# Kernel optimization log

Measured on AMD Instinct MI355X. Metric: run time of the kernel, lower is better.

The kernel has to match this reference:

```python
import jax, jax.numpy as jnp
import numpy as np


def setup_inputs() -> dict:
    key = jax.random.key(0)
    k1, k2, k3 = jax.random.split(key, 3)
    B, T, H = 64, 512, 1024
    return {
        "encoder_out": jax.random.normal(k1, (B, T, H), dtype=jnp.float32),
        "W_ih": jax.random.normal(k2, (3 * H, H), dtype=jnp.float32) * (1.0 / np.sqrt(H)),
        "W_hh": jax.random.normal(k3, (3 * H, H), dtype=jnp.float32) * (1.0 / np.sqrt(H)),
        "b_ih": jnp.zeros((3 * H,), dtype=jnp.float32),
        "b_hh": jnp.zeros((3 * H,), dtype=jnp.float32),
    }


def reference(encoder_out, W_ih, W_hh, b_ih, b_hh):
    # PyTorch GRUCell semantics; gate order in stacked weights is (r, z, n).
    B, T, H = encoder_out.shape

    # Batch the input-to-hidden projection across all timesteps: [B,T,3H]
    x_proj = jnp.einsum("bth,gh->btg", encoder_out, W_ih) + b_ih
    x_proj_t = jnp.swapaxes(x_proj, 0, 1)  # [T, B, 3H] for scan

    W_hh_T = W_hh.T  # [H, 3H]

    def step(h, xp):
        # recurrent projection: [B, 3H]
        h_proj = h @ W_hh_T + b_hh
        xr, xz, xn = jnp.split(xp, 3, axis=-1)
        hr, hz, hn = jnp.split(h_proj, 3, axis=-1)
        r = jax.nn.sigmoid(xr + hr)
        z = jax.nn.sigmoid(xz + hz)
        n = jnp.tanh(xn + r * hn)
        h_new = (1.0 - z) * n + z * h
        return h_new, h_new

    h0 = jnp.zeros((B, H), dtype=encoder_out.dtype)
    _, h_seq = jax.lax.scan(step, h0, x_proj_t)  # [T, B, H]
    return jnp.swapaxes(h_seq, 0, 1)  # [B, T, H]
```

## Files before the change

### kernel.cpp

```cpp
#include <hip/hip_runtime.h>
#include <hip/hip_bf16.h>


typedef short bf16x8 __attribute__((ext_vector_type(8)));
typedef float f32x4 __attribute__((ext_vector_type(4)));

#define NB 64
#define NT 512
#define NH 1024
#define NG 3072

static __device__ __forceinline__ float bf2f(unsigned short u) {
    unsigned int x = ((unsigned int)u) << 16;
    float f;
    __builtin_memcpy(&f, &x, sizeof(f));
    return f;
}
static __device__ __forceinline__ unsigned short f2bf(float f) {
    unsigned int x;
    __builtin_memcpy(&x, &f, sizeof(x));
    x += 0x7fffu + ((x >> 16) & 1u);
    return (unsigned short)(x >> 16);
}

static __device__ __forceinline__ f32x4 mfma16(bf16x8 a, bf16x8 b, f32x4 c) {
    return __builtin_amdgcn_mfma_f32_16x16x32_bf16(a, b, c, 0, 0, 0);
}

#define GLD16(gp, lp) __builtin_amdgcn_global_load_lds( \
    (const __attribute__((address_space(1))) void*)(gp), \
    (__attribute__((address_space(3))) void*)(lp), 16, 0, 0)

__global__ void k_fill_sentinel(float* __restrict__ o, long n) {
    long i = (long)blockIdx.x * blockDim.x + threadIdx.x;
    if (i < n) o[i] = 12345.0f;
}

__global__ void k_convert(const float* __restrict__ in, unsigned short* __restrict__ o, int n) {
    int i = blockIdx.x * blockDim.x + threadIdx.x;
    if (i < n) o[i] = f2bf(in[i]);
}

__global__ void k_convert_enc(const float* __restrict__ enc, unsigned short* __restrict__ o) {
    long i = (long)blockIdx.x * blockDim.x + threadIdx.x;
    if (i >= (long)NB * NT * NH) return;
    int h = (int)(i % NH);
    long bt = i / NH;
    int t = (int)(bt % NT);
    int b = (int)(bt / NT);
    o[((long)t * NB + b) * NH + h] = f2bf(enc[i]);
}

#define SYNC_WORDS (4 * NB * NH / 2 + 128)
__global__ void k_init_sync(unsigned int* __restrict__ base) {
    int i = blockIdx.x * blockDim.x + threadIdx.x;
    if (i < SYNC_WORDS) base[i] = 0u;
}

__global__ __launch_bounds__(256) void k_xproj(
    const unsigned short* __restrict__ X,
    const unsigned short* __restrict__ W,
    const float* __restrict__ bias,
    unsigned short* __restrict__ xp)
{
    __shared__ unsigned short As[128 * 32];
    __shared__ unsigned short Bs[128 * 32];

    const int tid  = threadIdx.x;
    const int lane = tid & 63;
    const int wv   = tid >> 6;
    const int l16  = lane & 15;
    const int lq   = lane >> 4;
    const int wr   = wv >> 1;
    const int wc   = wv & 1;
    const int n0   = blockIdx.x * 128;
    const int m0   = blockIdx.y * 128;

    f32x4 acc[4][4];
#pragma unroll
    for (int mi = 0; mi < 4; ++mi)
#pragma unroll
        for (int nj = 0; nj < 4; ++nj) acc[mi][nj] = (f32x4){0.f, 0.f, 0.f, 0.f};

    const int r0 = tid >> 2;
    const int c0e = (tid & 3) * 8;
    const int r1 = (256 + tid) >> 2;

    for (int k0 = 0; k0 < NH; k0 += 32) {
        GLD16(X + (size_t)(m0 + r0) * NH + k0 + c0e, &As[tid * 8]);
        GLD16(X + (size_t)(m0 + r1) * NH + k0 + c0e, &As[(256 + tid) * 8]);
        GLD16(W + (size_t)(n0 + r0) * NH + k0 + c0e, &Bs[tid * 8]);
        GLD16(W + (size_t)(n0 + r1) * NH + k0 + c0e, &Bs[(256 + tid) * 8]);
        __syncthreads();

        bf16x8 a[4], b[4];
#pragma unroll
        for (int mi = 0; mi < 4; ++mi)
            a[mi] = *(const bf16x8*)&As[(wr * 64 + mi * 16 + l16) * 32 + lq * 8];
#pragma unroll
        for (int nj = 0; nj < 4; ++nj)
            b[nj] = *(const bf16x8*)&Bs[(wc * 64 + nj * 16 + l16) * 32 + lq * 8];
#pragma unroll
        for (int mi = 0; mi < 4; ++mi)
#pragma unroll
            for (int nj = 0; nj < 4; ++nj)
                acc[mi][nj] = mfma16(a[mi], b[nj], acc[mi][nj]);
        __syncthreads();
    }

#pragma unroll
    for (int nj = 0; nj < 4; ++nj) {
        int n = n0 + wc * 64 + nj * 16 + l16;
        float bv = bias[n];
        int g   = n >> 10;
        int u   = n & 1023;
        int ugb = u >> 5;
        int ui  = u & 31;
#pragma unroll
        for (int mi = 0; mi < 4; ++mi) {
#pragma unroll
            for (int i = 0; i < 4; ++i) {
                int m = m0 + wr * 64 + mi * 16 + lq * 4 + i;
                int t = m >> 6;
                int b = m & 63;
                xp[(((long)t * 32 + ugb) * 64 + b) * 96 + g * 32 + ui] = f2bf(acc[mi][nj][i] + bv);
            }
        }
    }
}

__global__ __launch_bounds__(512, 1) void k_scan(
    const unsigned short* __restrict__ Whh,
    const float* __restrict__ bhh,
    const unsigned short* __restrict__ xp,
    unsigned short* __restrict__ hring,
    unsigned* __restrict__ flags,
    float* __restrict__ out)
{
    const int tid  = threadIdx.x;
    const int lane = tid & 63;
    const int wv   = tid >> 6;
    const int l16  = lane & 15;
    const int lq   = lane >> 4;
    const int bid  = blockIdx.x;
    const int mg   = bid >> 5;
    const int ug   = bid & 31;
    const int m0   = mg * 16;
    const int u0   = ug * 32;
    const int kc0  = wv * 128;

    bf16x8 Bf[3][2][4];
#pragma unroll
    for (int g = 0; g < 3; ++g)
#pragma unroll
        for (int f = 0; f < 2; ++f)
#pragma unroll
            for (int ks = 0; ks < 4; ++ks)
                Bf[g][f][ks] = *(const bf16x8*)(Whh + (long)(g * NH + u0 + f * 16 + l16) * NH + kc0 + ks * 32 + lq * 8);
#pragma unroll
    for (int g = 0; g < 3; ++g)
#pragma unroll
        for (int f = 0; f < 2; ++f)
#pragma unroll
            for (int ks = 0; ks < 4; ++ks)
                asm volatile("" : "+v"(Bf[g][f][ks]));

    const int u_loc = tid & 31;
    const int b_loc = tid >> 5;
    const int b_own = m0 + b_loc;
    const int u_own = u0 + u_loc;
    float bh[3];
#pragma unroll
    for (int g = 0; g < 3; ++g) bh[g] = bhh[g * NH + u_own];
    float hf = 0.0f;

    const int lane_t = (b_loc >> 2) * 16 + (u_loc & 15);
    const int i_t    = b_loc & 3;
    const int shalf  = (u_loc >> 4) * 3;

    __shared__ f32x4 red[8][6][64];

    for (int t = 0; t < NT; ++t) {
        const int slot_r = (t + 3) & 3;
        const int slot_w = t & 3;

        const unsigned short* xpp = xp + (((long)t * 32 + ug) * 64 + b_own) * 96;
        float xr = bf2f(xpp[u_loc]);
        float xz = bf2f(xpp[32 + u_loc]);
        float xn = bf2f(xpp[64 + u_loc]);

        if (t > 0) {
            if (wv == 0) {
                const unsigned* fp = flags + mg * 32 + (lane & 31);
                for (;;) {
                    unsigned fv;
                    asm volatile("global_load_dword %0, %1, off sc0 sc1\n\ts_waitcnt vmcnt(0)"
                                 : "=v"(fv) : "v"(fp) : "memory");
                    if (__all(fv >= (unsigned)t)) break;
                }
            }
            __syncthreads();
        }

        const unsigned short* hp = hring + ((slot_r * NB + m0 + l16) * NH + kc0 + lq * 8);
        bf16x8 av[4];
        asm volatile(
            "global_load_dwordx4 %0, %4, off sc0 sc1\n\t"
            "global_load_dwordx4 %1, %4, off offset:64 sc0 sc1\n\t"
            "global_load_dwordx4 %2, %4, off offset:128 sc0 sc1\n\t"
            "global_load_dwordx4 %3, %4, off offset:192 sc0 sc1\n\t"
            "s_waitcnt vmcnt(0)"
            : "=&v"(av[0]), "=&v"(av[1]), "=&v"(av[2]), "=&v"(av[3])
            : "v"(hp) : "memory");

        f32x4 acc[2][3];
#pragma unroll
        for (int f = 0; f < 2; ++f)
#pragma unroll
            for (int g = 0; g < 3; ++g) acc[f][g] = (f32x4){0.f, 0.f, 0.f, 0.f};
#pragma unroll
        for (int ks = 0; ks < 4; ++ks)
#pragma unroll
            for (int f = 0; f < 2; ++f)
#pragma unroll
                for (int g = 0; g < 3; ++g)
                    acc[f][g] = mfma16(av[ks], Bf[g][f][ks], acc[f][g]);

#pragma unroll
        for (int f = 0; f < 2; ++f)
#pragma unroll
            for (int g = 0; g < 3; ++g) red[wv][f * 3 + g][lane] = acc[f][g];
        __syncthreads();

        float pre[3];
#pragma unroll
        for (int g = 0; g < 3; ++g) {
            float s = 0.0f;
#pragma unroll
            for (int w = 0; w < 8; ++w) s += red[w][shalf + g][lane_t][i_t];
            pre[g] = s + bh[g];
        }

        float r = 1.0f / (1.0f + __expf(-(xr + pre[0])));
        float z = 1.0f / (1.0f + __expf(-(xz + pre[1])));
        float narg = xn + r * pre[2];
        float nval = 1.0f - 2.0f / (__expf(2.0f * narg) + 1.0f);
        float hnew = (1.0f - z) * nval + z * hf;
        hf = hnew;

        {
            unsigned short* hw = hring + (slot_w * NB + b_own) * NH + u_own;
            unsigned hv = (unsigned)f2bf(hnew);
            asm volatile("global_store_short %0, %1, off sc0 sc1"
                         :: "v"(hw), "v"(hv) : "memory");
        }
        asm volatile("s_waitcnt vmcnt(0)" ::: "memory");
        __syncthreads();
        if (tid == 0) {
            unsigned fv = (unsigned)(t + 1);
            asm volatile("global_store_dword %0, %1, off sc0 sc1"
                         :: "v"(flags + mg * 32 + ug), "v"(fv) : "memory");
        }
        out[((long)b_own * NT + t) * NH + u_own] = hnew;
    }
}

extern "C" void kernel_launch(void* const* d_in, const int* in_sizes, int n_in,
                              void* d_out, int out_size, void* d_ws, size_t ws_size,
                              hipStream_t stream) {
    const float* enc = (const float*)d_in[0];
    const float* Wih = (const float*)d_in[1];
    const float* Whh = (const float*)d_in[2];
    const float* bih = (const float*)d_in[3];
    const float* bhh = (const float*)d_in[4];
    float* out = (float*)d_out;

    char* p = (char*)d_ws;
    unsigned short* enc_t = (unsigned short*)p; p += (size_t)NT * NB * NH * 2;
    unsigned short* xp    = (unsigned short*)p; p += (size_t)NT * NB * NG * 2;
    unsigned short* wih_b = (unsigned short*)p; p += (size_t)NG * NH * 2;
    unsigned short* whh_b = (unsigned short*)p; p += (size_t)NG * NH * 2;
    size_t need = (size_t)(p - (char*)d_ws);

    unsigned short* hring = enc_t;
    unsigned* flags = (unsigned*)(hring + (size_t)4 * NB * NH);

    if (ws_size < need) {
        long n = (long)out_size;
        k_fill_sentinel<<<(int)((n + 255) / 256), 256, 0, stream>>>(out, n);
        return;
    }

    {
        int n = NG * NH;
        k_convert<<<(n + 255) / 256, 256, 0, stream>>>(Wih, wih_b, n);
        k_convert<<<(n + 255) / 256, 256, 0, stream>>>(Whh, whh_b, n);
        long ne = (long)NB * NT * NH;
        k_convert_enc<<<(int)((ne + 255) / 256), 256, 0, stream>>>(enc, enc_t);
    }

    {
        dim3 grid(NG / 128, (NT * NB) / 128);
        k_xproj<<<grid, 256, 0, stream>>>(enc_t, wih_b, bih, xp);
    }

    k_init_sync<<<(SYNC_WORDS + 255) / 256, 256, 0, stream>>>((unsigned*)hring);

    k_scan<<<128, 512, 0, stream>>>(whh_b, bhh, xp, hring, flags, out);
}
```

Before: 2.307 ms.

## Fuse input projection into the scan kernel and overlap it via per-tile flags

Launches one kernel of 256 blocks. The first 128 blocks compute the input projection, reading fp32 encoder data straight from memory and converting it to bf16 in place, then raise a per-tile done flag. The other 128 blocks run the recurrent scan and poll those flags before consuming each timestep. This removes the separate encoder transpose/convert pass and the xproj launch, and lets the projection overlap the latency-bound recurrence. The cost is that projection blocks use a smaller 128x128 tile with single-buffered LDS and no reuse across repeats. Correctness also depends on both block groups being resident at the same time, since the scan blocks spin on flags.

```diff
diff --git a/kernel.cpp b/kernel.cpp
--- a/kernel.cpp
+++ b/kernel.cpp
@@ -41,113 +41,123 @@
     if (i < n) o[i] = f2bf(in[i]);
 }
 
-__global__ void k_convert_enc(const float* __restrict__ enc, unsigned short* __restrict__ o) {
-    long i = (long)blockIdx.x * blockDim.x + threadIdx.x;
-    if (i >= (long)NB * NT * NH) return;
-    int h = (int)(i % NH);
-    long bt = i / NH;
-    int t = (int)(bt % NT);
-    int b = (int)(bt / NT);
-    o[((long)t * NB + b) * NH + h] = f2bf(enc[i]);
-}
-
-#define SYNC_WORDS (4 * NB * NH / 2 + 128)
+#define SYNC_WORDS (4 * NB * NH / 2 + 128 + 256)
 __global__ void k_init_sync(unsigned int* __restrict__ base) {
     int i = blockIdx.x * blockDim.x + threadIdx.x;
     if (i < SYNC_WORDS) base[i] = 0u;
 }
 
-__global__ __launch_bounds__(256) void k_xproj(
-    const unsigned short* __restrict__ X,
-    const unsigned short* __restrict__ W,
-    const float* __restrict__ bias,
-    unsigned short* __restrict__ xp)
-{
-    __shared__ unsigned short As[128 * 32];
-    __shared__ unsigned short Bs[128 * 32];
-
-    const int tid  = threadIdx.x;
-    const int lane = tid & 63;
-    const int wv   = tid >> 6;
-    const int l16  = lane & 15;
-    const int lq   = lane >> 4;
-    const int wr   = wv >> 1;
-    const int wc   = wv & 1;
-    const int n0   = blockIdx.x * 128;
-    const int m0   = blockIdx.y * 128;
-
-    f32x4 acc[4][4];
-#pragma unroll
-    for (int mi = 0; mi < 4; ++mi)
-#pragma unroll
-        for (int nj = 0; nj < 4; ++nj) acc[mi][nj] = (f32x4){0.f, 0.f, 0.f, 0.f};
-
-    const int r0 = tid >> 2;
-    const int c0e = (tid & 3) * 8;
-    const int r1 = (256 + tid) >> 2;
-
-    for (int k0 = 0; k0 < NH; k0 += 32) {
-        GLD16(X + (size_t)(m0 + r0) * NH + k0 + c0e, &As[tid * 8]);
-        GLD16(X + (size_t)(m0 + r1) * NH + k0 + c0e, &As[(256 + tid) * 8]);
-        GLD16(W + (size_t)(n0 + r0) * NH + k0 + c0e, &Bs[tid * 8]);
-        GLD16(W + (size_t)(n0 + r1) * NH + k0 + c0e, &Bs[(256 + tid) * 8]);
-        __syncthreads();
-
-        bf16x8 a[4], b[4];
-#pragma unroll
-        for (int mi = 0; mi < 4; ++mi)
-            a[mi] = *(const bf16x8*)&As[(wr * 64 + mi * 16 + l16) * 32 + lq * 8];
-#pragma unroll
-        for (int nj = 0; nj < 4; ++nj)
-            b[nj] = *(const bf16x8*)&Bs[(wc * 64 + nj * 16 + l16) * 32 + lq * 8];
-#pragma unroll
-        for (int mi = 0; mi < 4; ++mi)
-#pragma unroll
-            for (int nj = 0; nj < 4; ++nj)
-                acc[mi][nj] = mfma16(a[mi], b[nj], acc[mi][nj]);
-        __syncthreads();
-    }
-
-#pragma unroll
-    for (int nj = 0; nj < 4; ++nj) {
-        int n = n0 + wc * 64 + nj * 16 + l16;
-        float bv = bias[n];
-        int g   = n >> 10;
-        int u   = n & 1023;
-        int ugb = u >> 5;
-        int ui  = u & 31;
-#pragma unroll
-        for (int mi = 0; mi < 4; ++mi) {
-#pragma unroll
-            for (int i = 0; i < 4; ++i) {
-                int m = m0 + wr * 64 + mi * 16 + lq * 4 + i;
-                int t = m >> 6;
-                int b = m & 63;
-                xp[(((long)t * 32 + ugb) * 64 + b) * 96 + g * 32 + ui] = f2bf(acc[mi][nj][i] + bv);
-            }
-        }
-    }
-}
-
-__global__ __launch_bounds__(512, 1) void k_scan(
+__global__ __launch_bounds__(512, 1) void k_fused(
+    const unsigned short* __restrict__ Wih,
     const unsigned short* __restrict__ Whh,
+    const float* __restrict__ bih,
     const float* __restrict__ bhh,
-    const unsigned short* __restrict__ xp,
+    const float* __restrict__ enc,
+    unsigned short* __restrict__ xp,
     unsigned short* __restrict__ hring,
     unsigned* __restrict__ flags,
+    unsigned* __restrict__ xpdone,
     float* __restrict__ out)
 {
+    __shared__ char lds_raw[49152];
+
     const int tid  = threadIdx.x;
     const int lane = tid & 63;
     const int wv   = tid >> 6;
     const int l16  = lane & 15;
     const int lq   = lane >> 4;
     const int bid  = blockIdx.x;
-    const int mg   = bid >> 5;
-    const int ug   = bid & 31;
-    const int m0   = mg * 16;
-    const int u0   = ug * 32;
-    const int kc0  = wv * 128;
+
+    if (bid < 128) {
+        unsigned short* As = (unsigned short*)lds_raw;
+        unsigned short* Bs = (unsigned short*)(lds_raw + 8192);
+        const int wr = wv >> 2;
+        const int wc = wv & 3;
+        const int r  = tid >> 2;
+        const int ce = (tid & 3) * 8;
+
+        for (int rep = 0; rep < 2; ++rep) {
+            const int mt = bid + rep * 128;
+            const int m0 = mt * 128;
+            const int ma = m0 + r;
+            const float* agp = enc + ((size_t)(ma & 63) * NT + (ma >> 6)) * NH + ce;
+
+            for (int nt = 0; nt < 24; ++nt) {
+                const int n0 = nt * 128;
+                f32x4 acc[4][2];
+#pragma unroll
+                for (int mi = 0; mi < 4; ++mi)
+#pragma unroll
+                    for (int nj = 0; nj < 2; ++nj) acc[mi][nj] = (f32x4){0.f, 0.f, 0.f, 0.f};
+
+                for (int k0 = 0; k0 < NH; k0 += 32) {
+                    {
+                        float4 fa = *(const float4*)(agp + k0);
+                        float4 fb = *(const float4*)(agp + k0 + 4);
+                        union { unsigned short s[8]; bf16x8 v; } cv;
+                        cv.s[0] = f2bf(fa.x); cv.s[1] = f2bf(fa.y);
+                        cv.s[2] = f2bf(fa.z); cv.s[3] = f2bf(fa.w);
+                        cv.s[4] = f2bf(fb.x); cv.s[5] = f2bf(fb.y);
+                        cv.s[6] = f2bf(fb.z); cv.s[7] = f2bf(fb.w);
+                        *(bf16x8*)&As[r * 32 + ce] = cv.v;
+                    }
+                    GLD16(Wih + (size_t)(n0 + r) * NH + k0 + ce, &Bs[tid * 8]);
+                    __syncthreads();
+
+                    bf16x8 a[4], b[2];
+#pragma unroll
+                    for (int mi = 0; mi < 4; ++mi)
+                        a[mi] = *(const bf16x8*)&As[(wr * 64 + mi * 16 + l16) * 32 + lq * 8];
+#pragma unroll
+                    for (int nj = 0; nj < 2; ++nj)
+                        b[nj] = *(const bf16x8*)&Bs[(wc * 32 + nj * 16 + l16) * 32 + lq * 8];
+#pragma unroll
+                    for (int mi = 0; mi < 4; ++mi)
+#pragma unroll
+                        for (int nj = 0; nj < 2; ++nj)
+                            acc[mi][nj] = mfma16(a[mi], b[nj], acc[mi][nj]);
+                    __syncthreads();
+                }
+
+#pragma unroll
+                for (int nj = 0; nj < 2; ++nj) {
+                    int n = n0 + wc * 32 + nj * 16 + l16;
+                    float bv = bih[n];
+                    int g   = n >> 10;
+                    int u   = n & 1023;
+                    int ugb = u >> 5;
+                    int ui  = u & 31;
+#pragma unroll
+                    for (int mi = 0; mi < 4; ++mi) {
+#pragma unroll
+                        for (int i = 0; i < 4; ++i) {
+                            int m = m0 + wr * 64 + mi * 16 + lq * 4 + i;
+                            int t = m >> 6;
+                            int b = m & 63;
+                            xp[(((long)t * 32 + ugb) * 64 + b) * 96 + g * 32 + ui] =
+                                f2bf(acc[mi][nj][i] + bv);
+                        }
+                    }
+                }
+            }
+            __threadfence();
+            __syncthreads();
+            if (tid == 0) {
+                unsigned one = 1u;
+                asm volatile("global_store_dword %0, %1, off sc0 sc1"
+                             :: "v"(xpdone + mt), "v"(one) : "memory");
+            }
+        }
+        return;
+    }
+
+    f32x4 (*red)[6][64] = (f32x4(*)[6][64])lds_raw;
+    const int sb  = bid - 128;
+    const int mg  = sb >> 5;
+    const int ug  = sb & 31;
+    const int m0  = mg * 16;
+    const int u0  = ug * 32;
+    const int kc0 = wv * 128;
 
     bf16x8 Bf[3][2][4];
 #pragma unroll
@@ -178,40 +188,42 @@
     const int i_t    = b_loc & 3;
     const int shalf  = (u_loc >> 4) * 3;
 
-    __shared__ f32x4 red[8][6][64];
+    const unsigned* fp_h = flags + mg * 32 + wv * 4 + (lane & 3);
 
     for (int t = 0; t < NT; ++t) {
         const int slot_r = (t + 3) & 3;
         const int slot_w = t & 3;
 
-        const unsigned short* xpp = xp + (((long)t * 32 + ug) * 64 + b_own) * 96;
-        float xr = bf2f(xpp[u_loc]);
-        float xz = bf2f(xpp[32 + u_loc]);
-        float xn = bf2f(xpp[64 + u_loc]);
-
-        if (t > 0) {
-            if (wv == 0) {
-                const unsigned* fp = flags + mg * 32 + (lane & 31);
-                for (;;) {
-                    unsigned fv;
-                    asm volatile("global_load_dword %0, %1, off sc0 sc1\n\ts_waitcnt vmcnt(0)"
-                                 : "=v"(fv) : "v"(fp) : "memory");
-                    if (__all(fv >= (unsigned)t)) break;
-                }
+        {
+            const unsigned tgt = (lane < 4) ? (unsigned)t : 1u;
+            const unsigned* pp = (lane < 4) ? fp_h : (xpdone + (t >> 1));
+            for (;;) {
+                unsigned fv;
+                asm volatile("global_load_dword %0, %1, off sc0 sc1\n\ts_waitcnt vmcnt(0)"
+                             : "=v"(fv) : "v"(pp) : "memory");
+                if (__all(fv >= tgt)) break;
             }
-            __syncthreads();
-        }
-
+        }
+
+        const unsigned short* xaddr = xp + (((long)t * 32 + ug) * 64 + b_own) * 96 + u_loc;
         const unsigned short* hp = hring + ((slot_r * NB + m0 + l16) * NH + kc0 + lq * 8);
+        unsigned xv0, xv1, xv2;
         bf16x8 av[4];
         asm volatile(
-            "global_load_dwordx4 %0, %4, off sc0 sc1\n\t"
-            "global_load_dwordx4 %1, %4, off offset:64 sc0 sc1\n\t"
-            "global_load_dwordx4 %2, %4, off offset:128 sc0 sc1\n\t"
-            "global_load_dwordx4 %3, %4, off offset:192 sc0 sc1\n\t"
+            "global_load_ushort %0, %7, off sc0 sc1\n\t"
+            "global_load_ushort %1, %7, off offset:64 sc0 sc1\n\t"
+            "global_load_ushort %2, %7, off offset:128 sc0 sc1\n\t"
+            "global_load_dwordx4 %3, %8, off sc0 sc1\n\t"
+            "global_load_dwordx4 %4, %8, off offset:64 sc0 sc1\n\t"
+            "global_load_dwordx4 %5, %8, off offset:128 sc0 sc1\n\t"
+            "global_load_dwordx4 %6, %8, off offset:192 sc0 sc1\n\t"
             "s_waitcnt vmcnt(0)"
-            : "=&v"(av[0]), "=&v"(av[1]), "=&v"(av[2]), "=&v"(av[3])
-            : "v"(hp) : "memory");
+            : "=&v"(xv0), "=&v"(xv1), "=&v"(xv2),
+              "=&v"(av[0]), "=&v"(av[1]), "=&v"(av[2]), "=&v"(av[3])
+            : "v"(xaddr), "v"(hp) : "memory");
+        float xr = bf2f((unsigned short)xv0);
+        float xz = bf2f((unsigned short)xv1);
+        float xn = bf2f((unsigned short)xv2);
 
         f32x4 acc[2][3];
 #pragma unroll
@@ -276,14 +288,13 @@
     float* out = (float*)d_out;
 
     char* p = (char*)d_ws;
-    unsigned short* enc_t = (unsigned short*)p; p += (size_t)NT * NB * NH * 2;
     unsigned short* xp    = (unsigned short*)p; p += (size_t)NT * NB * NG * 2;
     unsigned short* wih_b = (unsigned short*)p; p += (size_t)NG * NH * 2;
     unsigned short* whh_b = (unsigned short*)p; p += (size_t)NG * NH * 2;
+    unsigned short* hring = (unsigned short*)p; p += (size_t)4 * NB * NH * 2;
+    unsigned* flags  = (unsigned*)p; p += 128 * 4;
+    unsigned* xpdone = (unsigned*)p; p += 256 * 4;
     size_t need = (size_t)(p - (char*)d_ws);
-
-    unsigned short* hring = enc_t;
-    unsigned* flags = (unsigned*)(hring + (size_t)4 * NB * NH);
 
     if (ws_size < need) {
         long n = (long)out_size;
@@ -295,16 +306,9 @@
         int n = NG * NH;
         k_convert<<<(n + 255) / 256, 256, 0, stream>>>(Wih, wih_b, n);
         k_convert<<<(n + 255) / 256, 256, 0, stream>>>(Whh, whh_b, n);
-        long ne = (long)NB * NT * NH;
-        k_convert_enc<<<(int)((ne + 255) / 256), 256, 0, stream>>>(enc, enc_t);
+        k_init_sync<<<(SYNC_WORDS + 255) / 256, 256, 0, stream>>>((unsigned*)hring);
     }
 
-    {
-        dim3 grid(NG / 128, (NT * NB) / 128);
-        k_xproj<<<grid, 256, 0, stream>>>(enc_t, wih_b, bih, xp);
-    }
-
-    k_init_sync<<<(SYNC_WORDS + 255) / 256, 256, 0, stream>>>((unsigned*)hring);
-
-    k_scan<<<128, 512, 0, stream>>>(whh_b, bhh, xp, hring, flags, out);
-}
+    k_fused<<<256, 512, 0, stream>>>(wih_b, whh_b, bih, bhh, enc,
+                                     xp, hring, flags, xpdone, out);
+}
```

New measurement: 3.241 ms. 40.5% more time.
